# Performance work log

Measured on AMD Instinct MI355X. Metric: run time of the kernel, lower is better.

Reference implementation:

```python
import jax, jax.numpy as jnp
import numpy as np

EMBED = 1024
HEADS = 16
HEAD_DIM = EMBED // HEADS
WINDOW = 256

def _linear(x, W, b):
    # torch nn.Linear: y = x @ W.T + b, W shape (out, in)
    return jnp.einsum('bse,oe->bso', x, W) + b

def setup_inputs() -> dict:
    key = jax.random.key(0)
    ks = jax.random.split(key, 16)
    B, S = 2, 2048
    std = 1.0 / np.sqrt(EMBED)
    d = {
        'query': jax.random.normal(ks[0], (B, S, EMBED), jnp.float32),
        'key':   jax.random.normal(ks[1], (B, S, EMBED), jnp.float32),
        'value': jax.random.normal(ks[2], (B, S, EMBED), jnp.float32),
        'Wq': jax.random.normal(ks[3], (EMBED, EMBED), jnp.float32) * std,
        'bq': jnp.zeros((EMBED,), jnp.float32),
        'Wk': jax.random.normal(ks[4], (EMBED, EMBED), jnp.float32) * std,
        'bk': jnp.zeros((EMBED,), jnp.float32),
        'Wv': jax.random.normal(ks[5], (EMBED, EMBED), jnp.float32) * std,
        'bv': jnp.zeros((EMBED,), jnp.float32),
        'Wo': jax.random.normal(ks[6], (EMBED, EMBED), jnp.float32) * std,
        'bo': jnp.zeros((EMBED,), jnp.float32),
    }
    return d

def reference(query, key, value, Wq, bq, Wk, bk, Wv, bv, Wo, bo):
    B, S, E = query.shape
    q = _linear(query, Wq, bq)
    k = _linear(key, Wk, bk)
    v = _linear(value, Wv, bv)
    # (B, H, S, D)
    q = q.reshape(B, S, HEADS, HEAD_DIM).transpose(0, 2, 1, 3)
    k = k.reshape(B, S, HEADS, HEAD_DIM).transpose(0, 2, 1, 3)
    v = v.reshape(B, S, HEADS, HEAD_DIM).transpose(0, 2, 1, 3)
    scale = 1.0 / jnp.sqrt(jnp.asarray(HEAD_DIM, q.dtype))
    scores = jnp.einsum('bhqd,bhkd->bhqk', q, k) * scale
    # Faithful local masking: mask is 0 inside window [i-w//2, i+w//2], 1 outside,
    # and is ADDED to scores (as in the source, not -inf fill).
    i = jnp.arange(S)[:, None]
    j = jnp.arange(S)[None, :]
    half = WINDOW // 2
    band = (jnp.abs(i - j) <= half)
    add_mask = jnp.where(band, 0.0, 1.0).astype(scores.dtype)  # (S, S)
    scores = scores + add_mask[None, None, :, :]
    attn = jax.nn.softmax(scores, axis=-1)  # dropout = identity (eval)
    out = jnp.einsum('bhqk,bhkd->bhqd', attn, v)
    out = out.transpose(0, 2, 1, 3).reshape(B, S, E)
    return _linear(out, Wo, bo)
```

## Files before the change

### kernel.cpp

```cpp
#include <hip/hip_runtime.h>
#include <stdint.h>

#define B_ 2
#define S_ 2048
#define E_ 1024
#define H_ 16
#define D_ 64
#define M_ (B_*S_)
#define PROJ_ ((size_t)M_*E_)
#define HALF_W 128

typedef float    f32x4 __attribute__((ext_vector_type(4)));
typedef short    s16x4 __attribute__((ext_vector_type(4)));
typedef short    s16x8 __attribute__((ext_vector_type(8)));
typedef __bf16   bf16x8 __attribute__((ext_vector_type(8)));
typedef _Float16 f16x8 __attribute__((ext_vector_type(8)));
typedef unsigned int u32x4 __attribute__((ext_vector_type(4)));

typedef const __attribute__((address_space(1))) void* gas_t;
typedef __attribute__((address_space(3))) void*       las_t;

__device__ __forceinline__ void gl16(const void* g, void* l) {
    __builtin_amdgcn_global_load_lds((gas_t)g, (las_t)l, 16, 0, 0);
}

__device__ __forceinline__ f32x4 MFMA(bf16x8 a, bf16x8 b, f32x4 c) {
    return __builtin_amdgcn_mfma_f32_16x16x32_bf16(a, b, c, 0, 0, 0);
}
__device__ __forceinline__ f32x4 MFMAH(f16x8 a, f16x8 b, f32x4 c) {
    return __builtin_amdgcn_mfma_f32_16x16x32_f16(a, b, c, 0, 0, 0);
}

__device__ __forceinline__ float fexp2(float x) {
    return __builtin_amdgcn_exp2f(x);
}

__device__ __forceinline__ unsigned short f2bf(float f) {
    union { float f; unsigned int u; } x; x.f = f;
    unsigned int u = x.u + 0x7FFFu + ((x.u >> 16) & 1u);
    return (unsigned short)(u >> 16);
}

__device__ __forceinline__ s16x8 cvt8(f32x4 a, f32x4 b) {
    s16x8 h;
    h[0]=(short)f2bf(a[0]); h[1]=(short)f2bf(a[1]); h[2]=(short)f2bf(a[2]); h[3]=(short)f2bf(a[3]);
    h[4]=(short)f2bf(b[0]); h[5]=(short)f2bf(b[1]); h[6]=(short)f2bf(b[2]); h[7]=(short)f2bf(b[3]);
    return h;
}

__global__ __launch_bounds__(256) void cvt_kernel(
    const float* __restrict__ q, const float* __restrict__ k, const float* __restrict__ v,
    const float* __restrict__ Wq, const float* __restrict__ Wk,
    const float* __restrict__ Wv, const float* __restrict__ Wo,
    unsigned short* __restrict__ xq, unsigned short* __restrict__ xk,
    unsigned short* __restrict__ xv, unsigned short* __restrict__ wbf)
{
    const int z = blockIdx.y;
    if (z >= 3 && blockIdx.x >= 512) return;
    const float* src; unsigned short* dst;
    switch (z) {
        case 0: src = q;  dst = xq; break;
        case 1: src = k;  dst = xk; break;
        case 2: src = v;  dst = xv; break;
        case 3: src = Wq; dst = wbf; break;
        case 4: src = Wk; dst = wbf + (size_t)E_*E_; break;
        case 5: src = Wv; dst = wbf + 2*(size_t)E_*E_; break;
        default: src = Wo; dst = wbf + 3*(size_t)E_*E_; break;
    }
    size_t i = ((size_t)blockIdx.x * 256 + threadIdx.x) * 8;
    f32x4 a = *(const f32x4*)(src + i);
    f32x4 c = *(const f32x4*)(src + i + 4);
    *(s16x8*)(dst + i) = cvt8(a, c);
}

__global__ __launch_bounds__(256, 3) void qkv_kernel(
    const unsigned short* __restrict__ xq, const unsigned short* __restrict__ xk,
    const unsigned short* __restrict__ xv,
    const unsigned short* __restrict__ wbf,
    const float* __restrict__ Wq, const float* __restrict__ Wk, const float* __restrict__ Wv,
    const float* __restrict__ bq, const float* __restrict__ bk, const float* __restrict__ bv,
    unsigned short* __restrict__ qkvout)
{
    const int z = blockIdx.z;
    const unsigned short* X  = (z==0) ? xq : (z==1) ? xk : xv;
    const float*          Wf = (z==0) ? Wq : (z==1) ? Wk : Wv;
    const float*        bias = (z==0) ? bq : (z==1) ? bk : bv;
    const unsigned short* Wb = wbf ? (wbf + (size_t)z * E_ * E_) : nullptr;
    unsigned short* dst = qkvout + (size_t)z * PROJ_;

    __shared__ __align__(16) unsigned short As[2][128 * 32];
    __shared__ __align__(16) unsigned short Bs[2][128 * 32];

    const int t = threadIdx.x;
    const int lane = t & 63, w = t >> 6;
    const int quad = lane >> 4, l16 = lane & 15;
    const int wo = (w & 1) * 64, wsb = (w >> 1) * 64;
    const int oBase = blockIdx.x * 128, sBase = blockIdx.y * 128;

    const int r0 = t >> 2;
    const int c4 = (t & 3) ^ (r0 & 3);
    const unsigned short* gX  = X + (size_t)(sBase + r0) * E_ + c4 * 8;
    const unsigned short* gWb = Wb ? Wb + (size_t)(oBase + r0) * E_ + c4 * 8 : nullptr;
    const float*          gWf = Wf + (size_t)(oBase + r0) * E_ + c4 * 8;

    f32x4 acc[4][4] = {};

    auto issue = [&](int kk, int pb) {
        unsigned short* dB = &Bs[pb][(size_t)w * 512];
        gl16(gX + kk, dB);
        gl16(gX + (size_t)64 * E_ + kk, dB + 2048);
        if (gWb) {
            unsigned short* dA = &As[pb][(size_t)w * 512];
            gl16(gWb + kk, dA);
            gl16(gWb + (size_t)64 * E_ + kk, dA + 2048);
        } else {
            const float* gp0 = gWf + kk;
            const float* gp1 = gWf + (size_t)64 * E_ + kk;
            f32x4 a0 = *(const f32x4*)gp0, a1 = *(const f32x4*)(gp0 + 4);
            f32x4 b0 = *(const f32x4*)gp1, b1 = *(const f32x4*)(gp1 + 4);
            *(s16x8*)&As[pb][(size_t)r0 * 32 + (t & 3) * 8]        = cvt8(a0, a1);
            *(s16x8*)&As[pb][(size_t)(r0 + 64) * 32 + (t & 3) * 8] = cvt8(b0, b1);
        }
    };

    issue(0, 0);
    __syncthreads();

    for (int s = 0; s < 32; s++) {
        const int pb = s & 1;
        if (s < 31) issue((s + 1) * 32, pb ^ 1);

        bf16x8 af[4], bfr[4];
        #pragma unroll
        for (int io = 0; io < 4; io++) {
            int r = wo + io * 16 + l16;
            af[io] = *(const bf16x8*)&As[pb][(size_t)r * 32 + ((quad ^ (l16 & 3)) * 8)];
        }
        #pragma unroll
        for (int is = 0; is < 4; is++) {
            int r = wsb + is * 16 + l16;
            bfr[is] = *(const bf16x8*)&Bs[pb][(size_t)r * 32 + ((quad ^ (l16 & 3)) * 8)];
        }
        #pragma unroll
        for (int io = 0; io < 4; io++)
            #pragma unroll
            for (int is = 0; is < 4; is++)
                acc[io][is] = MFMA(af[io], bfr[is], acc[io][is]);
        __syncthreads();
    }

    const float KSCL = 0.1803368801111204f;
    #pragma unroll
    for (int is = 0; is < 4; is++) {
        int sg = sBase + wsb + is * 16 + l16;
        int b = sg >> 11, sg2 = sg & 2047;
        int k6 = sg2 & 63;
        int slot = ((k6 >> 5) & 1) * 32 + ((k6 >> 2) & 3) * 8
                 + ((k6 >> 4) & 1) * 4 + (k6 & 3);
        #pragma unroll
        for (int io = 0; io < 4; io++) {
            int ocol0 = oBase + wo + io * 16 + quad * 4;
            f32x4 bias4 = *(const f32x4*)&bias[ocol0];
            int h = ocol0 >> 6, d0 = ocol0 & 63;
            size_t base = ((size_t)(b * H_ + h)) * ((size_t)S_ * D_);
            if (z == 0) {
                s16x4 h4;
                #pragma unroll
                for (int r = 0; r < 4; r++) h4[r] = (short)f2bf(acc[io][is][r] + bias4[r]);
                *(s16x4*)&dst[base + (size_t)sg2 * D_ + d0] = h4;
            } else if (z == 1) {
                s16x4 h4;
                #pragma unroll
                for (int r = 0; r < 4; r++)
                    h4[r] = (short)f2bf((acc[io][is][r] + bias4[r]) * KSCL);
                *(s16x4*)&dst[base + (size_t)sg2 * D_ + d0] = h4;
            } else {
                size_t vb = base + (size_t)(sg2 >> 6) * 4096 + (size_t)d0 * 64 + slot;
                #pragma unroll
                for (int r = 0; r < 4; r++) {
                    _Float16 hv = (_Float16)(acc[io][is][r] + bias4[r]);
                    dst[vb + (size_t)r * 64] = __builtin_bit_cast(unsigned short, hv);
                }
            }
        }
    }
}

__global__ __launch_bounds__(256, 4) void attn_kernel(
    const unsigned short* __restrict__ qkvout, unsigned short* __restrict__ attnout)
{
    const int bh = blockIdx.x, b = bh >> 4, h = bh & 15;
    const int qbase = blockIdx.y * 64;
    const int t = threadIdx.x, w = t >> 6, lane = t & 63;
    const int quad = lane >> 4, l16 = lane & 15;

    const unsigned short* qg = qkvout + (size_t)bh * (S_ * D_);
    const unsigned short* kg = qkvout + PROJ_ + (size_t)bh * (S_ * D_);
    const unsigned short* vT = qkvout + 2 * PROJ_ + (size_t)bh * (S_ * D_);

    __shared__ __align__(16) unsigned short Ks [2][64 * 64];
    __shared__ __align__(16) unsigned short VTs[2][64 * 64];

    const int qi = qbase + w * 16 + l16;
    bf16x8 aq0 = *(const bf16x8*)&qg[(size_t)qi * 64 + quad * 8];
    bf16x8 aq1 = *(const bf16x8*)&qg[(size_t)qi * 64 + 32 + quad * 8];

    f32x4 Oi[4] = {}, Oo[4] = {};
    f32x4 Si = {}, So = {};

    const int r0 = t >> 3;
    const int ch = ((t & 7) ^ (r0 & 7)) * 8;

    f16x8 onesv;
    #pragma unroll
    for (int j = 0; j < 8; j++) onesv[j] = (_Float16)1.0f;

    auto issue = [&](int kt, int pb) {
        unsigned short* dK = &Ks [pb][(size_t)w * 512];
        unsigned short* dV = &VTs[pb][(size_t)w * 512];
        gl16(kg + (size_t)(kt + r0) * 64 + ch,      dK);
        gl16(kg + (size_t)(kt + r0 + 32) * 64 + ch, dK + 2048);
        gl16(vT + (size_t)(kt + r0) * 64 + ch,      dV);
        gl16(vT + (size_t)(kt + r0 + 32) * 64 + ch, dV + 2048);
    };

    issue(0, 0);
    __syncthreads();

    #pragma unroll 2
    for (int s = 0; s < 32; s++) {
        const int pb = s & 1;
        const int kt = s * 64;
        if (s < 31) issue(kt + 64, pb ^ 1);

        const int dq = qbase - kt;
        const int adq = dq < 0 ? -dq : dq;
        const int cls = (adq <= 64) ? 0 : (adq >= 192 ? 1 : 2);

        f32x4 pp[4];
        const int sw = l16 & 7;
        #pragma unroll
        for (int sub = 0; sub < 4; sub++) {
            int row = sub * 16 + l16;
            bf16x8 bk0 = *(const bf16x8*)&Ks[pb][(size_t)row * 64 + ((quad ^ sw) * 8)];
            bf16x8 bk1 = *(const bf16x8*)&Ks[pb][(size_t)row * 64 + (((4 + quad) ^ sw) * 8)];
            f32x4 zz = {};
            zz = MFMA(bk0, aq0, zz);
            zz = MFMA(bk1, aq1, zz);
            if (cls == 2) {
                const int jb = kt + sub * 16 + quad * 4;
                #pragma unroll
                for (int r = 0; r < 4; r++) {
                    int di = qi - (jb + r); di = di < 0 ? -di : di;
                    pp[sub][r] = fexp2(zz[r] + (di <= HALF_W ? 0.f : 1.44269504089f));
                }
            } else {
                #pragma unroll
                for (int r = 0; r < 4; r++) pp[sub][r] = fexp2(zz[r]);
            }
        }

        u32x4 u0, u1;
        u0[0] = __builtin_bit_cast(unsigned int, __builtin_amdgcn_cvt_pkrtz(pp[0][0], pp[0][1]));
        u0[1] = __builtin_bit_cast(unsigned int, __builtin_amdgcn_cvt_pkrtz(pp[0][2], pp[0][3]));
        u0[2] = __builtin_bit_cast(unsigned int, __builtin_amdgcn_cvt_pkrtz(pp[1][0], pp[1][1]));
        u0[3] = __builtin_bit_cast(unsigned int, __builtin_amdgcn_cvt_pkrtz(pp[1][2], pp[1][3]));
        u1[0] = __builtin_bit_cast(unsigned int, __builtin_amdgcn_cvt_pkrtz(pp[2][0], pp[2][1]));
        u1[1] = __builtin_bit_cast(unsigned int, __builtin_amdgcn_cvt_pkrtz(pp[2][2], pp[2][3]));
        u1[2] = __builtin_bit_cast(unsigned int, __builtin_amdgcn_cvt_pkrtz(pp[3][0], pp[3][1]));
        u1[3] = __builtin_bit_cast(unsigned int, __builtin_amdgcn_cvt_pkrtz(pp[3][2], pp[3][3]));
        f16x8 aP0 = __builtin_bit_cast(f16x8, u0);
        f16x8 aP1 = __builtin_bit_cast(f16x8, u1);

        if (cls == 1) {
            #pragma unroll
            for (int dt = 0; dt < 4; dt++) {
                int row = dt * 16 + l16;
                f16x8 v0 = *(const f16x8*)&VTs[pb][(size_t)row * 64 + ((quad ^ sw) * 8)];
                f16x8 v1 = *(const f16x8*)&VTs[pb][(size_t)row * 64 + (((4 + quad) ^ sw) * 8)];
                Oo[dt] = MFMAH(aP0, v0, Oo[dt]);
                Oo[dt] = MFMAH(aP1, v1, Oo[dt]);
            }
            So = MFMAH(aP0, onesv, So);
            So = MFMAH(aP1, onesv, So);
        } else {
            #pragma unroll
            for (int dt = 0; dt < 4; dt++) {
                int row = dt * 16 + l16;
                f16x8 v0 = *(const f16x8*)&VTs[pb][(size_t)row * 64 + ((quad ^ sw) * 8)];
                f16x8 v1 = *(const f16x8*)&VTs[pb][(size_t)row * 64 + (((4 + quad) ^ sw) * 8)];
                Oi[dt] = MFMAH(aP0, v0, Oi[dt]);
                Oi[dt] = MFMAH(aP1, v1, Oi[dt]);
            }
            Si = MFMAH(aP0, onesv, Si);
            Si = MFMAH(aP1, onesv, Si);
        }
        __syncthreads();
    }

    const float E1 = 2.718281828459045f;
    float rd[4];
    #pragma unroll
    for (int r = 0; r < 4; r++) rd[r] = 1.0f / (Si[r] + E1 * So[r]);
    #pragma unroll
    for (int dt = 0; dt < 4; dt++)
        #pragma unroll
        for (int r = 0; r < 4; r++) {
            float oo = (Oi[dt][r] + E1 * Oo[dt][r]) * rd[r];
            int srow2 = qbase + w * 16 + quad * 4 + r;
            int col   = h * 64 + dt * 16 + l16;
            attnout[((size_t)(b * S_ + srow2)) * E_ + col] = f2bf(oo);
        }
}

__global__ __launch_bounds__(256, 4) void oproj_kernel(
    const unsigned short* __restrict__ Aattn, const unsigned short* __restrict__ WoBf,
    const float* __restrict__ Wo, const float* __restrict__ bo, float* __restrict__ out)
{
    __shared__ __align__(16) unsigned short As[2][64 * 32];
    __shared__ __align__(16) unsigned short Bs[2][64 * 32];

    const int t = threadIdx.x;
    const int lane = t & 63, w = t >> 6;
    const int quad = lane >> 4, l16 = lane & 15;
    const int wm = (w & 1) * 32, wn = (w >> 1) * 32;
    const int rowBase = blockIdx.y * 64, nBase = blockIdx.x * 64;

    const int r0 = t >> 2;
    const int c4 = (t & 3) ^ (r0 & 3);
    const unsigned short* gA  = Aattn + (size_t)(rowBase + r0) * E_ + c4 * 8;
    const unsigned short* gBb = WoBf ? WoBf + (size_t)(nBase + r0) * E_ + c4 * 8 : nullptr;
    const float*          gBf = Wo + (size_t)(nBase + r0) * E_ + c4 * 8;

    f32x4 acc[2][2] = {};

    auto issue = [&](int kk, int pb) {
        gl16(gA + kk, &As[pb][(size_t)w * 512]);
        if (gBb) {
            gl16(gBb + kk, &Bs[pb][(size_t)w * 512]);
        } else {
            const float* gp0 = gBf + kk;
            f32x4 a0 = *(const f32x4*)gp0, a1 = *(const f32x4*)(gp0 + 4);
            *(s16x8*)&Bs[pb][(size_t)r0 * 32 + (t & 3) * 8] = cvt8(a0, a1);
        }
    };

    issue(0, 0);
    __syncthreads();

    for (int s = 0; s < 32; s++) {
        const int pb = s & 1;
        if (s < 31) issue((s + 1) * 32, pb ^ 1);

        bf16x8 af[2], bfr[2];
        #pragma unroll
        for (int im = 0; im < 2; im++) {
            int r = wm + im * 16 + l16;
            af[im] = *(const bf16x8*)&As[pb][(size_t)r * 32 + ((quad ^ (l16 & 3)) * 8)];
        }
        #pragma unroll
        for (int in = 0; in < 2; in++) {
            int r = wn + in * 16 + l16;
            bfr[in] = *(const bf16x8*)&Bs[pb][(size_t)r * 32 + ((quad ^ (l16 & 3)) * 8)];
        }
        #pragma unroll
        for (int im = 0; im < 2; im++)
            #pragma unroll
            for (int in = 0; in < 2; in++)
                acc[im][in] = MFMA(af[im], bfr[in], acc[im][in]);
        __syncthreads();
    }

    #pragma unroll
    for (int im = 0; im < 2; im++)
      #pragma unroll
      for (int in = 0; in < 2; in++) {
          int col = nBase + wn + in * 16 + l16;
          float bb = bo[col];
          #pragma unroll
          for (int r = 0; r < 4; r++) {
              int row = rowBase + wm + im * 16 + quad * 4 + r;
              out[(size_t)row * E_ + col] = acc[im][in][r] + bb;
          }
      }
}

extern "C" void kernel_launch(void* const* d_in, const int* in_sizes, int n_in,
                              void* d_out, int out_size, void* d_ws, size_t ws_size,
                              hipStream_t stream) {
    const float* query = (const float*)d_in[0];
    const float* key_  = (const float*)d_in[1];
    const float* value = (const float*)d_in[2];
    const float* Wq = (const float*)d_in[3];
    const float* bq = (const float*)d_in[4];
    const float* Wk = (const float*)d_in[5];
    const float* bk = (const float*)d_in[6];
    const float* Wv = (const float*)d_in[7];
    const float* bv = (const float*)d_in[8];
    const float* Wo = (const float*)d_in[9];
    const float* bo = (const float*)d_in[10];

    unsigned short* ws      = (unsigned short*)d_ws;
    unsigned short* xv      = ws;
    unsigned short* attnout = ws;
    unsigned short* qkvout  = ws + PROJ_;
    size_t needW = (4 * PROJ_ + 4 * (size_t)E_ * E_) * 2;
    unsigned short* wbf = (ws_size >= needW) ? (ws + 4 * PROJ_) : nullptr;
    unsigned short* xq = (unsigned short*)d_out;
    unsigned short* xk = xq + PROJ_;

    cvt_kernel<<<dim3(2048, wbf ? 7 : 3), 256, 0, stream>>>(
        query, key_, value, Wq, Wk, Wv, Wo, xq, xk, xv, wbf);
    qkv_kernel<<<dim3(8, 32, 3), 256, 0, stream>>>(
        xq, xk, xv, wbf, Wq, Wk, Wv, bq, bk, bv, qkvout);
    attn_kernel<<<dim3(32, 32), 256, 0, stream>>>(qkvout, attnout);
    oproj_kernel<<<dim3(16, 64), 256, 0, stream>>>(
        attnout, wbf ? wbf + 3 * (size_t)E_ * E_ : nullptr, Wo, bo, (float*)d_out);
}
```

Baseline: 227.9 us.

## Fuse activation fp32-to-bf16 conversion into QKV GEMM loads

The separate conversion pass over query/key/value is removed. The QKV kernel now reads fp32 activations through registers, converts them with packed v_cvt_pk_bf16_f32 instructions, and writes them to LDS after the MFMA loop, so the next tile's loads overlap compute. This avoids one full round trip of the activations through global memory. The cost is that each activation tile is re-read in fp32 by the 8 column blocks (twice the bytes of bf16) and there is extra register pressure. The conversion rounding changes to the hardware instruction's behaviour.

```diff
diff --git a/kernel.cpp b/kernel.cpp
--- a/kernel.cpp
+++ b/kernel.cpp
@@ -48,25 +48,26 @@
     return h;
 }
 
+__device__ __forceinline__ unsigned int pkbf(float lo, float hi) {
+    unsigned int r;
+    asm("v_cvt_pk_bf16_f32 %0, %1, %2" : "=v"(r) : "v"(lo), "v"(hi));
+    return r;
+}
+__device__ __forceinline__ s16x8 pk8(f32x4 a, f32x4 b) {
+    u32x4 u;
+    u[0] = pkbf(a[0], a[1]); u[1] = pkbf(a[2], a[3]);
+    u[2] = pkbf(b[0], b[1]); u[3] = pkbf(b[2], b[3]);
+    return __builtin_bit_cast(s16x8, u);
+}
+
 __global__ __launch_bounds__(256) void cvt_kernel(
-    const float* __restrict__ q, const float* __restrict__ k, const float* __restrict__ v,
     const float* __restrict__ Wq, const float* __restrict__ Wk,
     const float* __restrict__ Wv, const float* __restrict__ Wo,
-    unsigned short* __restrict__ xq, unsigned short* __restrict__ xk,
-    unsigned short* __restrict__ xv, unsigned short* __restrict__ wbf)
+    unsigned short* __restrict__ wbf)
 {
     const int z = blockIdx.y;
-    if (z >= 3 && blockIdx.x >= 512) return;
-    const float* src; unsigned short* dst;
-    switch (z) {
-        case 0: src = q;  dst = xq; break;
-        case 1: src = k;  dst = xk; break;
-        case 2: src = v;  dst = xv; break;
-        case 3: src = Wq; dst = wbf; break;
-        case 4: src = Wk; dst = wbf + (size_t)E_*E_; break;
-        case 5: src = Wv; dst = wbf + 2*(size_t)E_*E_; break;
-        default: src = Wo; dst = wbf + 3*(size_t)E_*E_; break;
-    }
+    const float* src = (z==0) ? Wq : (z==1) ? Wk : (z==2) ? Wv : Wo;
+    unsigned short* dst = wbf + (size_t)z * E_ * E_;
     size_t i = ((size_t)blockIdx.x * 256 + threadIdx.x) * 8;
     f32x4 a = *(const f32x4*)(src + i);
     f32x4 c = *(const f32x4*)(src + i + 4);
@@ -74,15 +75,15 @@
 }
 
 __global__ __launch_bounds__(256, 3) void qkv_kernel(
-    const unsigned short* __restrict__ xq, const unsigned short* __restrict__ xk,
-    const unsigned short* __restrict__ xv,
+    const float* __restrict__ qf, const float* __restrict__ kf,
+    const float* __restrict__ vf,
     const unsigned short* __restrict__ wbf,
     const float* __restrict__ Wq, const float* __restrict__ Wk, const float* __restrict__ Wv,
     const float* __restrict__ bq, const float* __restrict__ bk, const float* __restrict__ bv,
     unsigned short* __restrict__ qkvout)
 {
     const int z = blockIdx.z;
-    const unsigned short* X  = (z==0) ? xq : (z==1) ? xk : xv;
+    const float*          Xf = (z==0) ? qf : (z==1) ? kf : vf;
     const float*          Wf = (z==0) ? Wq : (z==1) ? Wk : Wv;
     const float*        bias = (z==0) ? bq : (z==1) ? bk : bv;
     const unsigned short* Wb = wbf ? (wbf + (size_t)z * E_ * E_) : nullptr;
@@ -99,16 +100,24 @@
 
     const int r0 = t >> 2;
     const int c4 = (t & 3) ^ (r0 & 3);
-    const unsigned short* gX  = X + (size_t)(sBase + r0) * E_ + c4 * 8;
+    const float*          gXf = Xf + (size_t)(sBase + r0) * E_ + c4 * 8;
     const unsigned short* gWb = Wb ? Wb + (size_t)(oBase + r0) * E_ + c4 * 8 : nullptr;
     const float*          gWf = Wf + (size_t)(oBase + r0) * E_ + c4 * 8;
 
     f32x4 acc[4][4] = {};
-
-    auto issue = [&](int kk, int pb) {
-        unsigned short* dB = &Bs[pb][(size_t)w * 512];
-        gl16(gX + kk, dB);
-        gl16(gX + (size_t)64 * E_ + kk, dB + 2048);
+    f32x4 xa0, xa1, xb0, xb1;
+
+    auto loadX = [&](int kk) {
+        const float* p0 = gXf + kk;
+        const float* p1 = gXf + (size_t)64 * E_ + kk;
+        xa0 = *(const f32x4*)p0; xa1 = *(const f32x4*)(p0 + 4);
+        xb0 = *(const f32x4*)p1; xb1 = *(const f32x4*)(p1 + 4);
+    };
+    auto storeX = [&](int pb) {
+        *(s16x8*)&Bs[pb][(size_t)r0 * 32 + (t & 3) * 8]        = pk8(xa0, xa1);
+        *(s16x8*)&Bs[pb][(size_t)(r0 + 64) * 32 + (t & 3) * 8] = pk8(xb0, xb1);
+    };
+    auto stageW = [&](int kk, int pb) {
         if (gWb) {
             unsigned short* dA = &As[pb][(size_t)w * 512];
             gl16(gWb + kk, dA);
@@ -118,17 +127,22 @@
             const float* gp1 = gWf + (size_t)64 * E_ + kk;
             f32x4 a0 = *(const f32x4*)gp0, a1 = *(const f32x4*)(gp0 + 4);
             f32x4 b0 = *(const f32x4*)gp1, b1 = *(const f32x4*)(gp1 + 4);
-            *(s16x8*)&As[pb][(size_t)r0 * 32 + (t & 3) * 8]        = cvt8(a0, a1);
-            *(s16x8*)&As[pb][(size_t)(r0 + 64) * 32 + (t & 3) * 8] = cvt8(b0, b1);
+            *(s16x8*)&As[pb][(size_t)r0 * 32 + (t & 3) * 8]        = pk8(a0, a1);
+            *(s16x8*)&As[pb][(size_t)(r0 + 64) * 32 + (t & 3) * 8] = pk8(b0, b1);
         }
     };
 
-    issue(0, 0);
+    loadX(0);
+    stageW(0, 0);
+    storeX(0);
     __syncthreads();
 
     for (int s = 0; s < 32; s++) {
         const int pb = s & 1;
-        if (s < 31) issue((s + 1) * 32, pb ^ 1);
+        if (s < 31) {
+            loadX((s + 1) * 32);
+            stageW((s + 1) * 32, pb ^ 1);
+        }
 
         bf16x8 af[4], bfr[4];
         #pragma unroll
@@ -146,6 +160,8 @@
             #pragma unroll
             for (int is = 0; is < 4; is++)
                 acc[io][is] = MFMA(af[io], bfr[is], acc[io][is]);
+
+        if (s < 31) storeX(pb ^ 1);
         __syncthreads();
     }
 
@@ -401,18 +417,15 @@
     const float* bo = (const float*)d_in[10];
 
     unsigned short* ws      = (unsigned short*)d_ws;
-    unsigned short* xv      = ws;
     unsigned short* attnout = ws;
     unsigned short* qkvout  = ws + PROJ_;
     size_t needW = (4 * PROJ_ + 4 * (size_t)E_ * E_) * 2;
     unsigned short* wbf = (ws_size >= needW) ? (ws + 4 * PROJ_) : nullptr;
-    unsigned short* xq = (unsigned short*)d_out;
-    unsigned short* xk = xq + PROJ_;
-
-    cvt_kernel<<<dim3(2048, wbf ? 7 : 3), 256, 0, stream>>>(
-        query, key_, value, Wq, Wk, Wv, Wo, xq, xk, xv, wbf);
+
+    if (wbf)
+        cvt_kernel<<<dim3(512, 4), 256, 0, stream>>>(Wq, Wk, Wv, Wo, wbf);
     qkv_kernel<<<dim3(8, 32, 3), 256, 0, stream>>>(
-        xq, xk, xv, wbf, Wq, Wk, Wv, bq, bk, bv, qkvout);
+        query, key_, value, wbf, Wq, Wk, Wv, bq, bk, bv, qkvout);
     attn_kernel<<<dim3(32, 32), 256, 0, stream>>>(qkvout, attnout);
     oproj_kernel<<<dim3(16, 64), 256, 0, stream>>>(
         attnout, wbf ? wbf + 3 * (size_t)E_ * E_ : nullptr, Wo, bo, (float*)d_out);
```

Result: slower. 235.8 us (+3.4%).
